# Performance work log

Measured on AMD Instinct MI355X. Metric: run time of the kernel, lower is better.

The kernel has to match this reference:

```python
import jax, jax.numpy as jnp
import numpy as np

B, CIN, T = 64, 64, 4096
F, K = 128, 64


def setup_inputs() -> dict:
    key = jax.random.key(0)
    k1, k2, k3, k4, k5 = jax.random.split(key, 5)
    x = jax.random.normal(k1, (B, CIN, T), dtype=jnp.float32)
    conv_weights = jax.random.normal(k2, (F, K), dtype=jnp.float32) * 0.2
    spat_weights = jax.random.normal(k3, (F, CIN), dtype=jnp.float32) * 0.2
    weight = jax.random.normal(k4, (F,), dtype=jnp.float32)
    bias = jax.random.normal(k5, (F,), dtype=jnp.float32)
    return {"x": x, "conv_weights": conv_weights, "spat_weights": spat_weights,
            "weight": weight, "bias": bias}


def reference(x, conv_weights, spat_weights, weight, bias):
    n_filters, ksize = conv_weights.shape
    n_in = spat_weights.shape[1]
    # rank-1 merged kernel: [F, Cin, K]
    merged = conv_weights[:, None, :] * spat_weights[:, :, None]
    # valid conv1d: x [B,Cin,T] -> conved [B,F,T-K+1]
    conved = jax.lax.conv_general_dilated(
        x, merged, window_strides=(1,), padding='VALID',
        dimension_numbers=('NCH', 'OIH', 'NCH'))
    # per-filter weight norm
    norm_w = jnp.sqrt(jnp.sum(merged * merged, axis=(1, 2)))  # [F]
    # input norm: sliding-window sum of x^2 over channels and window
    sq = jnp.sum(x * x, axis=1, keepdims=True)  # [B,1,T]
    ones_k = jnp.ones((1, 1, ksize), dtype=x.dtype)
    slide = jax.lax.conv_general_dilated(
        sq, ones_k, window_strides=(1,), padding='VALID',
        dimension_numbers=('NCH', 'OIH', 'NCH'))[:, 0, :]  # [B,Tout]
    norm_inputs = jnp.sqrt(slide)
    scale = np.sqrt(n_in * ksize).astype(np.float32)
    cos_sims = conved / (norm_w[None, :, None] * norm_inputs[:, None, :]) * scale
    mean_cos = jnp.mean(jnp.abs(cos_sims), axis=2)  # [B,F]
    out_per_wave = mean_cos * weight[None, :] + bias[None, :]
    return jnp.sum(out_per_wave, axis=1)  # [B]
```

## Files before the change

kernel.cpp:

```cpp
#include <hip/hip_runtime.h>
#include <hip/hip_bf16.h>
#include <cstdint>
#include <cstddef>

#define BB   64
#define CINN 64
#define TS   4096
#define FF   128
#define KS   64
#define TOUT (TS - KS + 1)

#define TSEG 256
#define XROW 320
#define SXTW 35
#define YW   336
#define YWW  (YW / 2)

typedef __attribute__((ext_vector_type(8))) short short8;
typedef __attribute__((ext_vector_type(4))) float f32x4;
union FragU { unsigned int u[4]; short8 v; uint4 q4; };

static __device__ __forceinline__ unsigned int f2bf_u(float f) {
    __hip_bfloat16 h = __float2bfloat16(f);
    return (unsigned int)*reinterpret_cast<unsigned short*>(&h);
}

__global__ void k_band(const float* __restrict__ cw, const float* __restrict__ sw,
                       const float* __restrict__ weight,
                       uint4* __restrict__ bandB, float* __restrict__ wnf) {
    const int f = blockIdx.x, l = threadIdx.x;
    const int n = l & 15, q = l >> 4;
    for (int s = 0; s < 3; ++s) {
        FragU o;
#pragma unroll
        for (int i = 0; i < 4; ++i) {
            int i0 = 32 * s + 8 * q + 2 * i - n;
            int i1 = i0 + 1;
            float a = (i0 >= 0 && i0 < KS) ? cw[(size_t)f * KS + i0] : 0.f;
            float c = (i1 >= 0 && i1 < KS) ? cw[(size_t)f * KS + i1] : 0.f;
            o.u[i] = f2bf_u(a) | (f2bf_u(c) << 16);
        }
        bandB[((size_t)f * 3 + s) * 64 + l] = o.q4;
    }
    float a = sw[(size_t)f * CINN + l], c = cw[(size_t)f * KS + l];
    float v = a * a, u = c * c;
    for (int off = 32; off > 0; off >>= 1) {
        v += __shfl_down(v, off, 64);
        u += __shfl_down(u, off, 64);
    }
    if (l == 0) wnf[f] = weight[f] * rsqrtf(v * u) * (64.0f / (float)TOUT);
}

__global__ __launch_bounds__(1024, 4) void k_fused(
    const float* __restrict__ x, const float* __restrict__ sw,
    const uint4* __restrict__ bandB, const float* __restrict__ wnf,
    const float* __restrict__ bias, float* __restrict__ out)
{
    __shared__ unsigned int xT[XROW * SXTW];
    __shared__ unsigned int yL[FF * YWW];
    __shared__ float wred[16];

    const int tid = threadIdx.x;
    const int w = tid >> 6, l = tid & 63;
    const int b = blockIdx.y;
    const int t0 = blockIdx.x * TSEG;

    {
        const float* xb = x + (size_t)b * CINN * TS;
        float* sqp = (float*)yL;
        float4 s4a = {0.f, 0.f, 0.f, 0.f}, s4b = {0.f, 0.f, 0.f, 0.f};
#pragma unroll
        for (int r = 0; r < 2; ++r) {
            const int cp = w + 16 * r;
            const float* x0 = xb + (size_t)(2 * cp) * TS;
            {
                int p = t0 + 4 * l; if (p > TS - 4) p = TS - 4;
                float4 v0 = *(const float4*)(x0 + p);
                float4 v1 = *(const float4*)(x0 + TS + p);
                s4a.x += v0.x * v0.x + v1.x * v1.x;
                s4a.y += v0.y * v0.y + v1.y * v1.y;
                s4a.z += v0.z * v0.z + v1.z * v1.z;
                s4a.w += v0.w * v0.w + v1.w * v1.w;
                const int t = 4 * l;
                xT[(t + 0) * SXTW + cp] = f2bf_u(v0.x) | (f2bf_u(v1.x) << 16);
                xT[(t + 1) * SXTW + cp] = f2bf_u(v0.y) | (f2bf_u(v1.y) << 16);
                xT[(t + 2) * SXTW + cp] = f2bf_u(v0.z) | (f2bf_u(v1.z) << 16);
                xT[(t + 3) * SXTW + cp] = f2bf_u(v0.w) | (f2bf_u(v1.w) << 16);
            }
            if (l < 16) {
                int p = t0 + 256 + 4 * l; if (p > TS - 4) p = TS - 4;
                float4 v0 = *(const float4*)(x0 + p);
                float4 v1 = *(const float4*)(x0 + TS + p);
                s4b.x += v0.x * v0.x + v1.x * v1.x;
                s4b.y += v0.y * v0.y + v1.y * v1.y;
                s4b.z += v0.z * v0.z + v1.z * v1.z;
                s4b.w += v0.w * v0.w + v1.w * v1.w;
                const int t = 256 + 4 * l;
                xT[(t + 0) * SXTW + cp] = f2bf_u(v0.x) | (f2bf_u(v1.x) << 16);
                xT[(t + 1) * SXTW + cp] = f2bf_u(v0.y) | (f2bf_u(v1.y) << 16);
                xT[(t + 2) * SXTW + cp] = f2bf_u(v0.z) | (f2bf_u(v1.z) << 16);
                xT[(t + 3) * SXTW + cp] = f2bf_u(v0.w) | (f2bf_u(v1.w) << 16);
            }
        }
        *(float4*)(sqp + w * XROW + 4 * l) = s4a;
        if (l < 16) *(float4*)(sqp + w * XROW + 256 + 4 * l) = s4b;
    }
    __syncthreads();

    if (tid < XROW) {
        const float* sqp = (const float*)yL;
        float s = 0.f;
#pragma unroll
        for (int w2 = 0; w2 < 16; ++w2) s += sqp[w2 * XROW + tid];
        xT[tid * SXTW + 32] = __float_as_uint(s);
    }
    __syncthreads();

    const int m = l & 15, q = l >> 4;

    if (w == 0 && l < 32) {
        const int base = 8 * l;
        float s = 0.f, hd[8], tl[8];
#pragma unroll
        for (int k = 0; k < 64; ++k) {
            float v = __uint_as_float(xT[(base + k) * SXTW + 32]);
            if (k < 8) hd[k] = v;
            s += v;
        }
#pragma unroll
        for (int j = 0; j < 8; ++j) tl[j] = __uint_as_float(xT[(base + 64 + j) * SXTW + 32]);
        float rv[8];
#pragma unroll
        for (int j = 0; j < 8; ++j) {
            int tpos = t0 + base + j;
            rv[j] = (tpos < TOUT) ? rsqrtf(s) : 0.f;
            s += tl[j] - hd[j];
        }
#pragma unroll
        for (int j = 0; j < 8; ++j) {
            int t = base + j;
            xT[t * SXTW + 32 + ((t >> 6) & 1)] = __float_as_uint(rv[j]);
        }
    }

    {
        const int mw = w & 7, nh = w >> 3;
        short8 Af[2];
#pragma unroll
        for (int s = 0; s < 2; ++s) {
            const float* swr = sw + (size_t)(16 * mw + m) * CINN + s * 32 + q * 8;
            float4 w0 = *(const float4*)swr;
            float4 w1 = *(const float4*)(swr + 4);
            FragU fa;
            fa.u[0] = f2bf_u(w0.x) | (f2bf_u(w0.y) << 16);
            fa.u[1] = f2bf_u(w0.z) | (f2bf_u(w0.w) << 16);
            fa.u[2] = f2bf_u(w1.x) | (f2bf_u(w1.y) << 16);
            fa.u[3] = f2bf_u(w1.z) | (f2bf_u(w1.w) << 16);
            Af[s] = fa.v;
        }
        const bool evenl = (l & 1) == 0;
#pragma unroll
        for (int ti = 0; ti < 10; ++ti) {
            const int tt = nh * 10 + ti;
            const int t = tt * 16 + m;
            const int bw = t * SXTW + 4 * q;
            FragU b0, b1;
#pragma unroll
            for (int i = 0; i < 4; ++i) { b0.u[i] = xT[bw + i]; b1.u[i] = xT[bw + 16 + i]; }
            f32x4 acc = {0.f, 0.f, 0.f, 0.f};
            acc = __builtin_amdgcn_mfma_f32_16x16x32_bf16(Af[0], b0.v, acc, 0, 0, 0);
            acc = __builtin_amdgcn_mfma_f32_16x16x32_bf16(Af[1], b1.v, acc, 0, 0, 0);
#pragma unroll
            for (int r = 0; r < 4; ++r) {
                float o = __shfl_xor(acc[r], 1, 64);
                if (evenl) {
                    unsigned u = f2bf_u(acc[r]) | (f2bf_u(o) << 16);
                    yL[(16 * mw + 4 * q + r) * YWW + 8 * tt + (m >> 1)] = u;
                }
            }
        }
        yL[(tid >> 3) * YWW + 160 + (tid & 7)] = 0u;
    }
    __syncthreads();

    float rr[4];
#pragma unroll
    for (int r = 0; r < 4; ++r) {
        int t = 64 * q + 16 * r + m;
        rr[r] = __uint_as_float(xT[t * SXTW + 32 + (q & 1)]);
    }
    const int f0t = 8 * w;
    float acc = 0.f;
    uint4 pb0, pb1, pb2;
    {
        const uint4* bb = bandB + (size_t)f0t * 3 * 64;
        pb0 = bb[l]; pb1 = bb[64 + l]; pb2 = bb[128 + l];
    }
#pragma unroll 2
    for (int fi = 0; fi < 8; ++fi) {
        const int f = f0t + fi;
        FragU B0, B1, B2;
        B0.q4 = pb0; B1.q4 = pb1; B2.q4 = pb2;
        if (fi < 7) {
            const uint4* bb = bandB + (size_t)(f + 1) * 3 * 64;
            pb0 = bb[l]; pb1 = bb[64 + l]; pb2 = bb[128 + l];
        }
        const int abase = f * YWW + 8 * m + 4 * q;
        FragU a0, a1, a2;
        a0.q4 = *(const uint4*)(yL + abase);
        a1.q4 = *(const uint4*)(yL + abase + 16);
        a2.q4 = *(const uint4*)(yL + abase + 32);
        f32x4 d = {0.f, 0.f, 0.f, 0.f};
        d = __builtin_amdgcn_mfma_f32_16x16x32_bf16(a0.v, B0.v, d, 0, 0, 0);
        d = __builtin_amdgcn_mfma_f32_16x16x32_bf16(a1.v, B1.v, d, 0, 0, 0);
        d = __builtin_amdgcn_mfma_f32_16x16x32_bf16(a2.v, B2.v, d, 0, 0, 0);
        float facc = 0.f;
#pragma unroll
        for (int r = 0; r < 4; ++r) facc += fabsf(d[r]) * rr[r];
        acc += wnf[f] * facc;
    }

    for (int off = 32; off > 0; off >>= 1) acc += __shfl_down(acc, off, 64);
    if (l == 0) wred[w] = acc;
    __syncthreads();
    if (tid == 0) {
        float s = 0.f;
#pragma unroll
        for (int i = 0; i < 16; ++i) s += wred[i];
        atomicAdd(out + b, s);
    }
    if (blockIdx.x == 0 && tid < FF) {
        float v = bias[tid];
        for (int off = 32; off > 0; off >>= 1) v += __shfl_down(v, off, 64);
        if ((tid & 63) == 0) atomicAdd(out + b, v);
    }
}

__global__ __launch_bounds__(256) void k_naive(
    const float* __restrict__ x, const float* __restrict__ cw,
    const float* __restrict__ sw, const float* __restrict__ weight,
    const float* __restrict__ bias, float* __restrict__ out)
{
    __shared__ float yl[TS];
    __shared__ float ql[TS];
    __shared__ float wred[4];
    const int f = blockIdx.x, b = blockIdx.y, tid = threadIdx.x;
    for (int t = tid; t < TS; t += 256) {
        float a = 0.f, s = 0.f;
        for (int c = 0; c < CINN; ++c) {
            float v = x[((size_t)b * CINN + c) * TS + t];
            a += sw[(size_t)f * CINN + c] * v;
            s += v * v;
        }
        yl[t] = a; ql[t] = s;
    }
    __syncthreads();
    float acc = 0.f;
    for (int t = tid; t < TOUT; t += 256) {
        float cv = 0.f, sl = 0.f;
        for (int k = 0; k < KS; ++k) { cv += cw[(size_t)f * KS + k] * yl[t + k]; sl += ql[t + k]; }
        acc += fabsf(cv) * rsqrtf(sl);
    }
    float ssw = 0.f, scw = 0.f;
    for (int c = 0; c < CINN; ++c) { float v = sw[(size_t)f * CINN + c]; ssw += v * v; }
    for (int k = 0; k < KS; ++k)   { float v = cw[(size_t)f * KS + k];  scw += v * v; }
    const float wnf = weight[f] * rsqrtf(ssw * scw) * 64.0f / (float)TOUT;
    for (int off = 32; off > 0; off >>= 1) acc += __shfl_down(acc, off, 64);
    if ((tid & 63) == 0) wred[tid >> 6] = acc;
    __syncthreads();
    if (tid == 0) {
        float tot = (wred[0] + wred[1] + wred[2] + wred[3]) * wnf;
        if (f == 0) {
            float bsum = 0.f;
            for (int ff = 0; ff < FF; ++ff) bsum += bias[ff];
            tot += bsum;
        }
        atomicAdd(out + b, tot);
    }
}

extern "C" void kernel_launch(void* const* d_in, const int* in_sizes, int n_in,
                              void* d_out, int out_size, void* d_ws, size_t ws_size,
                              hipStream_t stream) {
    const float* x  = (const float*)d_in[0];
    const float* cw = (const float*)d_in[1];
    const float* sw = (const float*)d_in[2];
    const float* w  = (const float*)d_in[3];
    const float* bs = (const float*)d_in[4];
    float* out = (float*)d_out;

    hipMemsetAsync(d_out, 0, (size_t)out_size * sizeof(float), stream);

    const size_t bandBytes = (size_t)FF * 3 * 64 * 16;
    const size_t wnBytes   = (size_t)FF * sizeof(float);

    if (bandBytes + wnBytes <= ws_size) {
        uint4* bandB = (uint4*)d_ws;
        float* wnf   = (float*)((char*)d_ws + bandBytes);
        k_band <<<dim3(FF), 64, 0, stream>>>(cw, sw, w, bandB, wnf);
        k_fused<<<dim3(TS / TSEG, BB), 1024, 0, stream>>>(x, sw, bandB, wnf, bs, out);
    } else {
        k_naive<<<dim3(FF, BB), 256, 0, stream>>>(x, cw, sw, w, bs, out);
    }
}
```

Measured before the change: 151.0 us.

## Loop four time tiles per block with register prefetch and preformatted spatial fragments

Each block now processes four consecutive 256-sample time tiles in a loop instead of one. The next tile's x data is prefetched into registers while the current tile's second MFMA stage runs. Spatial-weight bf16 MFMA fragments are precomputed once in k_band and held in registers across tiles. The first-stage MFMA is reorganised so x is the A operand and each wave computes four filter groups per loaded x fragment, writing packed bf16 results directly without the lane shuffle. The grid shrinks from 16x64 to 4x64 blocks, which lowers block-launch and weight-conversion overhead but reduces parallelism and adds extra barriers per tile.

```diff
diff --git a/kernel.cpp b/kernel.cpp
--- a/kernel.cpp
+++ b/kernel.cpp
@@ -27,7 +27,8 @@
 
 __global__ void k_band(const float* __restrict__ cw, const float* __restrict__ sw,
                        const float* __restrict__ weight,
-                       uint4* __restrict__ bandB, float* __restrict__ wnf) {
+                       uint4* __restrict__ bandB, float* __restrict__ wnf,
+                       uint4* __restrict__ swF) {
     const int f = blockIdx.x, l = threadIdx.x;
     const int n = l & 15, q = l >> 4;
     for (int s = 0; s < 3; ++s) {
@@ -42,6 +43,18 @@
         }
         bandB[((size_t)f * 3 + s) * 64 + l] = o.q4;
     }
+    if ((f & 15) == 0) {
+        const int ft = f >> 4;
+        for (int s = 0; s < 2; ++s) {
+            FragU o;
+#pragma unroll
+            for (int i = 0; i < 4; ++i) {
+                const float* sr = sw + (size_t)(16 * ft + n) * CINN + 32 * s + 8 * q + 2 * i;
+                o.u[i] = f2bf_u(sr[0]) | (f2bf_u(sr[1]) << 16);
+            }
+            swF[((size_t)ft * 2 + s) * 64 + l] = o.q4;
+        }
+    }
     float a = sw[(size_t)f * CINN + l], c = cw[(size_t)f * KS + l];
     float v = a * a, u = c * c;
     for (int off = 32; off > 0; off >>= 1) {
@@ -52,7 +65,7 @@
 }
 
 __global__ __launch_bounds__(1024, 4) void k_fused(
-    const float* __restrict__ x, const float* __restrict__ sw,
+    const float* __restrict__ x, const uint4* __restrict__ swF,
     const uint4* __restrict__ bandB, const float* __restrict__ wnf,
     const float* __restrict__ bias, float* __restrict__ out)
 {
@@ -62,21 +75,47 @@
 
     const int tid = threadIdx.x;
     const int w = tid >> 6, l = tid & 63;
+    const int m = l & 15, q = l >> 4;
     const int b = blockIdx.y;
-    const int t0 = blockIdx.x * TSEG;
-
+    const int g = blockIdx.x;
+
+    const float* xb = x + (size_t)b * CINN * TS;
+
+    FragU swf[4][2];
     {
-        const float* xb = x + (size_t)b * CINN * TS;
-        float* sqp = (float*)yL;
-        float4 s4a = {0.f, 0.f, 0.f, 0.f}, s4b = {0.f, 0.f, 0.f, 0.f};
+        const int quad = w & 1;
+#pragma unroll
+        for (int fi = 0; fi < 4; ++fi)
+#pragma unroll
+            for (int s = 0; s < 2; ++s)
+                swf[fi][s].q4 = swF[((size_t)(4 * quad + fi) * 2 + s) * 64 + l];
+    }
+
+    float4 xa[2][2];
+    auto loadx = [&](int tb) {
 #pragma unroll
         for (int r = 0; r < 2; ++r) {
             const int cp = w + 16 * r;
             const float* x0 = xb + (size_t)(2 * cp) * TS;
-            {
-                int p = t0 + 4 * l; if (p > TS - 4) p = TS - 4;
-                float4 v0 = *(const float4*)(x0 + p);
-                float4 v1 = *(const float4*)(x0 + TS + p);
+            int p = tb + 4 * l; if (p > TS - 4) p = TS - 4;
+            xa[r][0] = *(const float4*)(x0 + p);
+            xa[r][1] = *(const float4*)(x0 + TS + p);
+        }
+    };
+    loadx(4 * g * TSEG);
+
+    float acc = 0.f;
+
+    for (int tile = 0; tile < 4; ++tile) {
+        const int t0 = (4 * g + tile) * TSEG;
+
+        {
+            float* sqp = (float*)yL;
+            float4 s4a = {0.f, 0.f, 0.f, 0.f}, s4b = {0.f, 0.f, 0.f, 0.f};
+#pragma unroll
+            for (int r = 0; r < 2; ++r) {
+                const int cp = w + 16 * r;
+                float4 v0 = xa[r][0], v1 = xa[r][1];
                 s4a.x += v0.x * v0.x + v1.x * v1.x;
                 s4a.y += v0.y * v0.y + v1.y * v1.y;
                 s4a.z += v0.z * v0.z + v1.z * v1.z;
@@ -88,136 +127,126 @@
                 xT[(t + 3) * SXTW + cp] = f2bf_u(v0.w) | (f2bf_u(v1.w) << 16);
             }
             if (l < 16) {
-                int p = t0 + 256 + 4 * l; if (p > TS - 4) p = TS - 4;
-                float4 v0 = *(const float4*)(x0 + p);
-                float4 v1 = *(const float4*)(x0 + TS + p);
-                s4b.x += v0.x * v0.x + v1.x * v1.x;
-                s4b.y += v0.y * v0.y + v1.y * v1.y;
-                s4b.z += v0.z * v0.z + v1.z * v1.z;
-                s4b.w += v0.w * v0.w + v1.w * v1.w;
-                const int t = 256 + 4 * l;
-                xT[(t + 0) * SXTW + cp] = f2bf_u(v0.x) | (f2bf_u(v1.x) << 16);
-                xT[(t + 1) * SXTW + cp] = f2bf_u(v0.y) | (f2bf_u(v1.y) << 16);
-                xT[(t + 2) * SXTW + cp] = f2bf_u(v0.z) | (f2bf_u(v1.z) << 16);
-                xT[(t + 3) * SXTW + cp] = f2bf_u(v0.w) | (f2bf_u(v1.w) << 16);
-            }
-        }
-        *(float4*)(sqp + w * XROW + 4 * l) = s4a;
-        if (l < 16) *(float4*)(sqp + w * XROW + 256 + 4 * l) = s4b;
-    }
-    __syncthreads();
-
-    if (tid < XROW) {
-        const float* sqp = (const float*)yL;
-        float s = 0.f;
-#pragma unroll
-        for (int w2 = 0; w2 < 16; ++w2) s += sqp[w2 * XROW + tid];
-        xT[tid * SXTW + 32] = __float_as_uint(s);
-    }
-    __syncthreads();
-
-    const int m = l & 15, q = l >> 4;
-
-    if (w == 0 && l < 32) {
-        const int base = 8 * l;
-        float s = 0.f, hd[8], tl[8];
-#pragma unroll
-        for (int k = 0; k < 64; ++k) {
-            float v = __uint_as_float(xT[(base + k) * SXTW + 32]);
-            if (k < 8) hd[k] = v;
-            s += v;
-        }
-#pragma unroll
-        for (int j = 0; j < 8; ++j) tl[j] = __uint_as_float(xT[(base + 64 + j) * SXTW + 32]);
-        float rv[8];
-#pragma unroll
-        for (int j = 0; j < 8; ++j) {
-            int tpos = t0 + base + j;
-            rv[j] = (tpos < TOUT) ? rsqrtf(s) : 0.f;
-            s += tl[j] - hd[j];
-        }
-#pragma unroll
-        for (int j = 0; j < 8; ++j) {
-            int t = base + j;
-            xT[t * SXTW + 32 + ((t >> 6) & 1)] = __float_as_uint(rv[j]);
-        }
-    }
-
-    {
-        const int mw = w & 7, nh = w >> 3;
-        short8 Af[2];
-#pragma unroll
-        for (int s = 0; s < 2; ++s) {
-            const float* swr = sw + (size_t)(16 * mw + m) * CINN + s * 32 + q * 8;
-            float4 w0 = *(const float4*)swr;
-            float4 w1 = *(const float4*)(swr + 4);
-            FragU fa;
-            fa.u[0] = f2bf_u(w0.x) | (f2bf_u(w0.y) << 16);
-            fa.u[1] = f2bf_u(w0.z) | (f2bf_u(w0.w) << 16);
-            fa.u[2] = f2bf_u(w1.x) | (f2bf_u(w1.y) << 16);
-            fa.u[3] = f2bf_u(w1.z) | (f2bf_u(w1.w) << 16);
-            Af[s] = fa.v;
-        }
-        const bool evenl = (l & 1) == 0;
-#pragma unroll
-        for (int ti = 0; ti < 10; ++ti) {
-            const int tt = nh * 10 + ti;
-            const int t = tt * 16 + m;
-            const int bw = t * SXTW + 4 * q;
-            FragU b0, b1;
-#pragma unroll
-            for (int i = 0; i < 4; ++i) { b0.u[i] = xT[bw + i]; b1.u[i] = xT[bw + 16 + i]; }
-            f32x4 acc = {0.f, 0.f, 0.f, 0.f};
-            acc = __builtin_amdgcn_mfma_f32_16x16x32_bf16(Af[0], b0.v, acc, 0, 0, 0);
-            acc = __builtin_amdgcn_mfma_f32_16x16x32_bf16(Af[1], b1.v, acc, 0, 0, 0);
+#pragma unroll
+                for (int r = 0; r < 2; ++r) {
+                    const int cp = w + 16 * r;
+                    const float* x0 = xb + (size_t)(2 * cp) * TS;
+                    int p = t0 + 256 + 4 * l; if (p > TS - 4) p = TS - 4;
+                    float4 v0 = *(const float4*)(x0 + p);
+                    float4 v1 = *(const float4*)(x0 + TS + p);
+                    s4b.x += v0.x * v0.x + v1.x * v1.x;
+                    s4b.y += v0.y * v0.y + v1.y * v1.y;
+                    s4b.z += v0.z * v0.z + v1.z * v1.z;
+                    s4b.w += v0.w * v0.w + v1.w * v1.w;
+                    const int t = 256 + 4 * l;
+                    xT[(t + 0) * SXTW + cp] = f2bf_u(v0.x) | (f2bf_u(v1.x) << 16);
+                    xT[(t + 1) * SXTW + cp] = f2bf_u(v0.y) | (f2bf_u(v1.y) << 16);
+                    xT[(t + 2) * SXTW + cp] = f2bf_u(v0.z) | (f2bf_u(v1.z) << 16);
+                    xT[(t + 3) * SXTW + cp] = f2bf_u(v0.w) | (f2bf_u(v1.w) << 16);
+                }
+            }
+            *(float4*)(sqp + w * XROW + 4 * l) = s4a;
+            if (l < 16) *(float4*)(sqp + w * XROW + 256 + 4 * l) = s4b;
+        }
+        __syncthreads();
+
+        if (tid < XROW) {
+            const float* sqp = (const float*)yL;
+            float s = 0.f;
+#pragma unroll
+            for (int w2 = 0; w2 < 16; ++w2) s += sqp[w2 * XROW + tid];
+            xT[tid * SXTW + 32] = __float_as_uint(s);
+        }
+        __syncthreads();
+
+        if (w == 15 && l < 32) {
+            const int base = 8 * l;
+            float s = 0.f, hd[8], tl[8];
+#pragma unroll
+            for (int k = 0; k < 64; ++k) {
+                float v = __uint_as_float(xT[(base + k) * SXTW + 32]);
+                if (k < 8) hd[k] = v;
+                s += v;
+            }
+#pragma unroll
+            for (int j = 0; j < 8; ++j) tl[j] = __uint_as_float(xT[(base + 64 + j) * SXTW + 32]);
+            float rv[8];
+#pragma unroll
+            for (int j = 0; j < 8; ++j) {
+                int tpos = t0 + base + j;
+                rv[j] = (tpos < TOUT) ? rsqrtf(s) : 0.f;
+                s += tl[j] - hd[j];
+            }
+#pragma unroll
+            for (int j = 0; j < 8; ++j) {
+                int t = base + j;
+                xT[t * SXTW + 32 + ((t >> 6) & 1)] = __float_as_uint(rv[j]);
+            }
+        }
+
+        {
+            const int quad = w & 1;
+            for (int tt = (w >> 1); tt < 20; tt += 8) {
+                const int bw = (16 * tt + m) * SXTW + 4 * q;
+                FragU b0, b1;
+#pragma unroll
+                for (int i = 0; i < 4; ++i) { b0.u[i] = xT[bw + i]; b1.u[i] = xT[bw + 16 + i]; }
+#pragma unroll
+                for (int fi = 0; fi < 4; ++fi) {
+                    f32x4 d = {0.f, 0.f, 0.f, 0.f};
+                    d = __builtin_amdgcn_mfma_f32_16x16x32_bf16(b0.v, swf[fi][0].v, d, 0, 0, 0);
+                    d = __builtin_amdgcn_mfma_f32_16x16x32_bf16(b1.v, swf[fi][1].v, d, 0, 0, 0);
+                    const int f = 16 * (4 * quad + fi) + m;
+                    uint2 o;
+                    o.x = f2bf_u(d[0]) | (f2bf_u(d[1]) << 16);
+                    o.y = f2bf_u(d[2]) | (f2bf_u(d[3]) << 16);
+                    *(uint2*)(yL + f * YWW + 8 * tt + 2 * q) = o;
+                }
+            }
+            yL[(tid >> 3) * YWW + 160 + (tid & 7)] = 0u;
+        }
+
+        if (tile < 3) loadx(t0 + TSEG);
+        __syncthreads();
+
+        {
+            float rr[4];
 #pragma unroll
             for (int r = 0; r < 4; ++r) {
-                float o = __shfl_xor(acc[r], 1, 64);
-                if (evenl) {
-                    unsigned u = f2bf_u(acc[r]) | (f2bf_u(o) << 16);
-                    yL[(16 * mw + 4 * q + r) * YWW + 8 * tt + (m >> 1)] = u;
+                int t = 64 * q + 16 * r + m;
+                rr[r] = __uint_as_float(xT[t * SXTW + 32 + (q & 1)]);
+            }
+            const int f0t = 8 * w;
+            uint4 pb0, pb1, pb2;
+            {
+                const uint4* bb = bandB + (size_t)f0t * 3 * 64;
+                pb0 = bb[l]; pb1 = bb[64 + l]; pb2 = bb[128 + l];
+            }
+#pragma unroll 2
+            for (int fi = 0; fi < 8; ++fi) {
+                const int f = f0t + fi;
+                FragU B0, B1, B2;
+                B0.q4 = pb0; B1.q4 = pb1; B2.q4 = pb2;
+                if (fi < 7) {
+                    const uint4* bb = bandB + (size_t)(f + 1) * 3 * 64;
+                    pb0 = bb[l]; pb1 = bb[64 + l]; pb2 = bb[128 + l];
                 }
-            }
-        }
-        yL[(tid >> 3) * YWW + 160 + (tid & 7)] = 0u;
-    }
-    __syncthreads();
-
-    float rr[4];
-#pragma unroll
-    for (int r = 0; r < 4; ++r) {
-        int t = 64 * q + 16 * r + m;
-        rr[r] = __uint_as_float(xT[t * SXTW + 32 + (q & 1)]);
-    }
-    const int f0t = 8 * w;
-    float acc = 0.f;
-    uint4 pb0, pb1, pb2;
-    {
-        const uint4* bb = bandB + (size_t)f0t * 3 * 64;
-        pb0 = bb[l]; pb1 = bb[64 + l]; pb2 = bb[128 + l];
-    }
-#pragma unroll 2
-    for (int fi = 0; fi < 8; ++fi) {
-        const int f = f0t + fi;
-        FragU B0, B1, B2;
-        B0.q4 = pb0; B1.q4 = pb1; B2.q4 = pb2;
-        if (fi < 7) {
-            const uint4* bb = bandB + (size_t)(f + 1) * 3 * 64;
-            pb0 = bb[l]; pb1 = bb[64 + l]; pb2 = bb[128 + l];
-        }
-        const int abase = f * YWW + 8 * m + 4 * q;
-        FragU a0, a1, a2;
-        a0.q4 = *(const uint4*)(yL + abase);
-        a1.q4 = *(const uint4*)(yL + abase + 16);
-        a2.q4 = *(const uint4*)(yL + abase + 32);
-        f32x4 d = {0.f, 0.f, 0.f, 0.f};
-        d = __builtin_amdgcn_mfma_f32_16x16x32_bf16(a0.v, B0.v, d, 0, 0, 0);
-        d = __builtin_amdgcn_mfma_f32_16x16x32_bf16(a1.v, B1.v, d, 0, 0, 0);
-        d = __builtin_amdgcn_mfma_f32_16x16x32_bf16(a2.v, B2.v, d, 0, 0, 0);
-        float facc = 0.f;
-#pragma unroll
-        for (int r = 0; r < 4; ++r) facc += fabsf(d[r]) * rr[r];
-        acc += wnf[f] * facc;
+                const int abase = f * YWW + 8 * m + 4 * q;
+                FragU a0, a1, a2;
+                a0.q4 = *(const uint4*)(yL + abase);
+                a1.q4 = *(const uint4*)(yL + abase + 16);
+                a2.q4 = *(const uint4*)(yL + abase + 32);
+                f32x4 d = {0.f, 0.f, 0.f, 0.f};
+                d = __builtin_amdgcn_mfma_f32_16x16x32_bf16(a0.v, B0.v, d, 0, 0, 0);
+                d = __builtin_amdgcn_mfma_f32_16x16x32_bf16(a1.v, B1.v, d, 0, 0, 0);
+                d = __builtin_amdgcn_mfma_f32_16x16x32_bf16(a2.v, B2.v, d, 0, 0, 0);
+                float facc = 0.f;
+#pragma unroll
+                for (int r = 0; r < 4; ++r) facc += fabsf(d[r]) * rr[r];
+                acc += wnf[f] * facc;
+            }
+        }
+        __syncthreads();
     }
 
     for (int off = 32; off > 0; off >>= 1) acc += __shfl_down(acc, off, 64);
@@ -229,7 +258,7 @@
         for (int i = 0; i < 16; ++i) s += wred[i];
         atomicAdd(out + b, s);
     }
-    if (blockIdx.x == 0 && tid < FF) {
+    if (g == 0 && tid < FF) {
         float v = bias[tid];
         for (int off = 32; off > 0; off >>= 1) v += __shfl_down(v, off, 64);
         if ((tid & 63) == 0) atomicAdd(out + b, v);
@@ -293,12 +322,14 @@
 
     const size_t bandBytes = (size_t)FF * 3 * 64 * 16;
     const size_t wnBytes   = (size_t)FF * sizeof(float);
-
-    if (bandBytes + wnBytes <= ws_size) {
+    const size_t swfBytes  = (size_t)(FF / 16) * 2 * 64 * 16;
+
+    if (bandBytes + wnBytes + swfBytes <= ws_size) {
         uint4* bandB = (uint4*)d_ws;
         float* wnf   = (float*)((char*)d_ws + bandBytes);
-        k_band <<<dim3(FF), 64, 0, stream>>>(cw, sw, w, bandB, wnf);
-        k_fused<<<dim3(TS / TSEG, BB), 1024, 0, stream>>>(x, sw, bandB, wnf, bs, out);
+        uint4* swF   = (uint4*)((char*)d_ws + bandBytes + wnBytes);
+        k_band <<<dim3(FF), 64, 0, stream>>>(cw, sw, w, bandB, wnf, swF);
+        k_fused<<<dim3(4, BB), 1024, 0, stream>>>(x, swF, bandB, wnf, bs, out);
     } else {
         k_naive<<<dim3(FF, BB), 256, 0, stream>>>(x, cw, sw, w, bs, out);
     }
```

Result: slower. 162.5 us (+7.6%).
